# Kernel optimization log

Measured on AMD Instinct MI355X. Metric: run time of the kernel, lower is better.

The kernel has to match this reference:

```python
import jax, jax.numpy as jnp
import numpy as np

BATCH = 2048
DIMS = [256, 256, 256, 128]  # input, hidden, hidden, output
N_ATOMS = 4  # identity, sin, tanh, square


def setup_inputs() -> dict:
    key = jax.random.key(0)
    ks = jax.random.split(key, 8)
    inp = {"x": jax.random.normal(ks[0], (BATCH, DIMS[0]), dtype=jnp.float32)}
    for li in range(3):
        out_d, in_d = DIMS[li + 1], DIMS[li]
        inp[f"W{li}"] = jax.random.normal(ks[1 + li], (out_d, in_d), dtype=jnp.float32) * 0.1
        inp[f"b{li}"] = jnp.zeros((out_d,), dtype=jnp.float32)
        inp[f"f_idx{li}"] = jax.random.randint(ks[4 + li], (out_d, in_d), 0, N_ATOMS, dtype=jnp.int32)
    return inp


def _w_eff(W, idx):
    # per-element atom nonlinearity selected by idx: [identity, sin, tanh, square]
    atoms = jnp.stack([W, jnp.sin(W), jnp.tanh(W), W * W], axis=0)  # [A, out, in]
    return jnp.take_along_axis(atoms, idx[None].astype(jnp.int32), axis=0)[0]


def reference(x, W0, b0, W1, b1, W2, b2, f_idx0, f_idx1, f_idx2):
    layers = [(W0, b0, f_idx0), (W1, b1, f_idx1), (W2, b2, f_idx2)]
    h = x
    n = len(layers)
    for li, (W, b, idx) in enumerate(layers):
        We = _w_eff(W, idx)                       # [out, in]
        z = h[:, None, :] * We[None, :, :]        # [batch, out, in]
        gz = z if li == n - 1 else jnp.tanh(z)    # g_fixed='tanh' on hidden layers
        h = gz.sum(axis=-1) + b[None, :]          # [batch, out]
    return h
```

## Files before the change

### kernel.cpp

```cpp
#include <hip/hip_runtime.h>
#include <math.h>


typedef float v2f __attribute__((ext_vector_type(2)));

#define SC   2.885390081777927f
#define INV  (1.0f / 2.885390081777927f)
#define INV2PI 0.15915494309189535f
#define HS_CLAMP 32.0f
#define C8   0.00390625f

__device__ __forceinline__ float fast_rcp(float x)  { return __builtin_amdgcn_rcpf(x); }
__device__ __forceinline__ float fast_exp2(float x) { return __builtin_amdgcn_exp2f(x); }
__device__ __forceinline__ v2f pk2(float a, float b) { v2f r; r.x = a; r.y = b; return r; }

__device__ __forceinline__ v2f pk_add(v2f a, v2f b) {
    v2f d; asm("v_pk_add_f32 %0, %1, %2" : "=v"(d) : "v"(a), "v"(b)); return d;
}
__device__ __forceinline__ v2f pk_mul(v2f a, v2f b) {
    v2f d; asm("v_pk_mul_f32 %0, %1, %2" : "=v"(d) : "v"(a), "v"(b)); return d;
}
__device__ __forceinline__ v2f pk_fma(v2f a, v2f b, v2f c) {
    v2f d; asm("v_pk_fma_f32 %0, %1, %2, %3" : "=v"(d) : "v"(a), "v"(b), "v"(c)); return d;
}
__device__ __forceinline__ v2f pk_fma_lo(v2f a, v2f s, v2f c) {
    v2f d; asm("v_pk_fma_f32 %0, %1, %2, %3 op_sel_hi:[1,0,1]"
               : "=v"(d) : "v"(a), "v"(s), "v"(c)); return d;
}
__device__ __forceinline__ v2f pk_fma_hi(v2f a, v2f s, v2f c) {
    v2f d; asm("v_pk_fma_f32 %0, %1, %2, %3 op_sel:[0,1,0] op_sel_hi:[1,1,1]"
               : "=v"(d) : "v"(a), "v"(s), "v"(c)); return d;
}
__device__ __forceinline__ v2f pk_exp(v2f t) {
    v2f e; e.x = fast_exp2(t.x); e.y = fast_exp2(t.y); return e;
}
__device__ __forceinline__ v2f lo2(float4 w) { return pk2(w.x, w.y); }
__device__ __forceinline__ v2f hi2(float4 w) { return pk2(w.z, w.w); }

__global__ void weff_kernel(const float* __restrict__ W0, const int* __restrict__ I0,
                            const float* __restrict__ W1, const int* __restrict__ I1,
                            const float* __restrict__ W2, const int* __restrict__ I2,
                            float* __restrict__ ws) {
    int tid = blockIdx.x * blockDim.x + threadIdx.x;
    const float* W; const int* I; float* out; int outd; int e;
    if (tid < 65536)        { W = W0; I = I0; out = ws;          outd = 256; e = tid; }
    else if (tid < 131072)  { W = W1; I = I1; out = ws + 65536;  outd = 256; e = tid - 65536; }
    else if (tid < 163840)  { W = W2; I = I2; out = ws + 131072; outd = 128; e = tid - 131072; }
    else return;
    int o = e >> 8;
    int i = e & 255;
    float w = W[e];
    int idx = I[e];
    float sn = __builtin_amdgcn_sinf(w * INV2PI);
    float th = 1.0f - 2.0f * fast_rcp(fast_exp2(w * SC) + 1.0f);
    float sq = w * w;
    float v = (idx == 1) ? sn : (idx == 2) ? th : (idx == 3) ? sq : w;
    out[(i >> 2) * (outd * 4) + o * 4 + (i & 3)] = v;
}

struct ND { v2f n, d; };
__device__ __forceinline__ ND tree4(float4 pa, float4 pb, float4 w, v2f m8, v2f c8) {
    v2f h0 = pk2(pa.x, pa.y), h1 = pk2(pa.z, pa.w);
    v2f h2 = pk2(pb.x, pb.y), h3 = pk2(pb.z, pb.w);
    v2f wxy = lo2(w), wzw = hi2(w);
    v2f B0 = pk_add(pk_exp(pk_fma_lo(h0, wxy, m8)), c8);
    v2f B1 = pk_add(pk_exp(pk_fma_hi(h1, wxy, m8)), c8);
    v2f B2 = pk_add(pk_exp(pk_fma_lo(h2, wzw, m8)), c8);
    v2f B3 = pk_add(pk_exp(pk_fma_hi(h3, wzw, m8)), c8);
    v2f S1 = pk_add(B0, B1), P1 = pk_mul(B0, B1);
    v2f S2 = pk_add(B2, B3), P2 = pk_mul(B2, B3);
    ND r;
    r.n = pk_fma(S2, P1, pk_mul(S1, P2));
    r.d = pk_mul(P1, P2);
    return r;
}

__device__ __forceinline__ v2f sig8_acc(ND a, ND b, v2f acc) {
    v2f num = pk_fma(b.n, a.d, pk_mul(a.n, b.d));
    v2f den = pk_mul(a.d, b.d);
    v2f rd;  rd.x = fast_rcp(den.x); rd.y = fast_rcp(den.y);
    return pk_fma(num, rd, acc);
}

__global__ __launch_bounds__(512, 8) void mlp_kernel(
    const float* __restrict__ x,  const float* __restrict__ b0,
    const float* __restrict__ b1, const float* __restrict__ b2,
    const float* __restrict__ ws, float* __restrict__ out) {
    const float4* We0 = (const float4*)ws;
    const float4* We1 = (const float4*)(ws + 65536);
    const float4* We2 = (const float4*)(ws + 131072);

    __shared__ __align__(16) v2f hA[256];
    __shared__ __align__(16) v2f hB[256];
    __shared__ __align__(16) v2f part[512];

    const int t = threadIdx.x;
    const int g = t >> 8;
    const int o = t & 255;
    const int row0 = blockIdx.x * 2;

    const v2f m8 = pk2(-8.0f, -8.0f);
    const v2f c8 = pk2(C8, C8);

    {
        float xv = x[(row0 + g) * 256 + o] * SC;
        xv = fminf(fmaxf(xv, -HS_CLAMP), HS_CLAMP);
        ((float*)(hA + o))[g] = xv;
    }
    __syncthreads();

    {
        v2f acc = pk2(0.f, 0.f);
#pragma unroll 2
        for (int icc = 0; icc < 32; icc += 2) {
            int ic = g * 32 + icc;
            float4 w0 = We0[ic * 256 + o];
            float4 w1 = We0[(ic + 1) * 256 + o];
            const float4* hp = (const float4*)(hA + ic * 4);
            ND r0 = tree4(hp[0], hp[1], w0, m8, c8);
            ND r1 = tree4(hp[2], hp[3], w1, m8, c8);
            acc = sig8_acc(r0, r1, acc);
        }
        part[g * 256 + o] = acc;
        __syncthreads();
        float s = ((const float*)(part + o))[g] + ((const float*)(part + 256 + o))[g];
        float h = (256.0f - 0.0078125f * s + b0[o]) * SC;
        h = fminf(fmaxf(h, -HS_CLAMP), HS_CLAMP);
        ((float*)(hB + o))[g] = h;
        __syncthreads();
    }

    {
        v2f acc = pk2(0.f, 0.f);
#pragma unroll 2
        for (int icc = 0; icc < 32; icc += 2) {
            int ic = g * 32 + icc;
            float4 w0 = We1[ic * 256 + o];
            float4 w1 = We1[(ic + 1) * 256 + o];
            const float4* hp = (const float4*)(hB + ic * 4);
            ND r0 = tree4(hp[0], hp[1], w0, m8, c8);
            ND r1 = tree4(hp[2], hp[3], w1, m8, c8);
            acc = sig8_acc(r0, r1, acc);
        }
        part[g * 256 + o] = acc;
        __syncthreads();
        float s = ((const float*)(part + o))[g] + ((const float*)(part + 256 + o))[g];
        float h = (256.0f - 0.0078125f * s + b1[o]) * SC;
        h = fminf(fmaxf(h, -HS_CLAMP), HS_CLAMP);
        ((float*)(hA + o))[g] = h;
        __syncthreads();
    }

    {
        const int o2 = t & 127;
        const int q  = t >> 7;
        v2f acc = pk2(0.f, 0.f);
#pragma unroll 4
        for (int icc = 0; icc < 16; icc++) {
            int ic = q * 16 + icc;
            float4 w = We2[ic * 128 + o2];
            const float4* hp = (const float4*)(hA + ic * 4);
            float4 pa = hp[0], pb = hp[1];
            v2f h0 = pk2(pa.x, pa.y), h1 = pk2(pa.z, pa.w);
            v2f h2 = pk2(pb.x, pb.y), h3 = pk2(pb.z, pb.w);
            v2f wxy = lo2(w), wzw = hi2(w);
            acc = pk_fma_lo(h0, wxy, acc);
            acc = pk_fma_hi(h1, wxy, acc);
            acc = pk_fma_lo(h2, wzw, acc);
            acc = pk_fma_hi(h3, wzw, acc);
        }
        part[q * 128 + o2] = acc;
        __syncthreads();
        if (t < 256) {
            int r = t >> 7, oo = t & 127;
            float s = ((const float*)(part + oo))[r]
                    + ((const float*)(part + 128 + oo))[r]
                    + ((const float*)(part + 256 + oo))[r]
                    + ((const float*)(part + 384 + oo))[r];
            out[(row0 + r) * 128 + oo] = s * INV + b2[oo];
        }
    }
}

extern "C" void kernel_launch(void* const* d_in, const int* in_sizes, int n_in,
                              void* d_out, int out_size, void* d_ws, size_t ws_size,
                              hipStream_t stream) {
    const float* x  = (const float*)d_in[0];
    const float* W0 = (const float*)d_in[1];
    const float* b0 = (const float*)d_in[2];
    const int*   I0 = (const int*)  d_in[3];
    const float* W1 = (const float*)d_in[4];
    const float* b1 = (const float*)d_in[5];
    const int*   I1 = (const int*)  d_in[6];
    const float* W2 = (const float*)d_in[7];
    const float* b2 = (const float*)d_in[8];
    const int*   I2 = (const int*)  d_in[9];
    float* ws  = (float*)d_ws;
    float* out = (float*)d_out;

    weff_kernel<<<640, 256, 0, stream>>>(W0, I0, W1, I1, W2, I2, ws);
    mlp_kernel<<<1024, 512, 0, stream>>>(x, b0, b1, b2, ws, out);
}
```

Baseline: 115.4 us.

## Process four rows per block to reuse weight loads across two row pairs

Each block now handles four batch rows instead of two. Every float4 of effective weights loaded from global memory is applied to both row pairs, with separate shared activation and partial-sum buffers for each pair. The grid is halved and the launch bound drops to four blocks per SM to leave room for the extra registers. This halves weight traffic per output, but it raises register pressure, lowers the number of resident waves and leaves fewer blocks to spread across CUs.

```diff
diff --git a/kernel.cpp b/kernel.cpp
--- a/kernel.cpp
+++ b/kernel.cpp
@@ -82,7 +82,7 @@
     return pk_fma(num, rd, acc);
 }
 
-__global__ __launch_bounds__(512, 8) void mlp_kernel(
+__global__ __launch_bounds__(512, 4) void mlp_kernel(
     const float* __restrict__ x,  const float* __restrict__ b0,
     const float* __restrict__ b1, const float* __restrict__ b2,
     const float* __restrict__ ws, float* __restrict__ out) {
@@ -90,14 +90,17 @@
     const float4* We1 = (const float4*)(ws + 65536);
     const float4* We2 = (const float4*)(ws + 131072);
 
-    __shared__ __align__(16) v2f hA[256];
-    __shared__ __align__(16) v2f hB[256];
-    __shared__ __align__(16) v2f part[512];
+    __shared__ __align__(16) v2f hA0[256];
+    __shared__ __align__(16) v2f hA1[256];
+    __shared__ __align__(16) v2f hB0[256];
+    __shared__ __align__(16) v2f hB1[256];
+    __shared__ __align__(16) v2f partA[512];
+    __shared__ __align__(16) v2f partB[512];
 
     const int t = threadIdx.x;
     const int g = t >> 8;
     const int o = t & 255;
-    const int row0 = blockIdx.x * 2;
+    const int row0 = blockIdx.x * 4;
 
     const v2f m8 = pk2(-8.0f, -8.0f);
     const v2f c8 = pk2(C8, C8);
@@ -105,80 +108,109 @@
     {
         float xv = x[(row0 + g) * 256 + o] * SC;
         xv = fminf(fmaxf(xv, -HS_CLAMP), HS_CLAMP);
-        ((float*)(hA + o))[g] = xv;
+        ((float*)&hA0[o])[g] = xv;
+        float xw = x[(row0 + 2 + g) * 256 + o] * SC;
+        xw = fminf(fmaxf(xw, -HS_CLAMP), HS_CLAMP);
+        ((float*)&hA1[o])[g] = xw;
     }
     __syncthreads();
 
     {
-        v2f acc = pk2(0.f, 0.f);
+        const float bias = b0[o];
+        v2f acc0 = pk2(0.f, 0.f), acc1 = pk2(0.f, 0.f);
 #pragma unroll 2
         for (int icc = 0; icc < 32; icc += 2) {
             int ic = g * 32 + icc;
             float4 w0 = We0[ic * 256 + o];
             float4 w1 = We0[(ic + 1) * 256 + o];
-            const float4* hp = (const float4*)(hA + ic * 4);
-            ND r0 = tree4(hp[0], hp[1], w0, m8, c8);
-            ND r1 = tree4(hp[2], hp[3], w1, m8, c8);
-            acc = sig8_acc(r0, r1, acc);
+            const float4* hp0 = (const float4*)(hA0 + ic * 4);
+            const float4* hp1 = (const float4*)(hA1 + ic * 4);
+            ND r0 = tree4(hp0[0], hp0[1], w0, m8, c8);
+            ND r1 = tree4(hp0[2], hp0[3], w1, m8, c8);
+            acc0 = sig8_acc(r0, r1, acc0);
+            ND r2 = tree4(hp1[0], hp1[1], w0, m8, c8);
+            ND r3 = tree4(hp1[2], hp1[3], w1, m8, c8);
+            acc1 = sig8_acc(r2, r3, acc1);
         }
-        part[g * 256 + o] = acc;
-        __syncthreads();
-        float s = ((const float*)(part + o))[g] + ((const float*)(part + 256 + o))[g];
-        float h = (256.0f - 0.0078125f * s + b0[o]) * SC;
-        h = fminf(fmaxf(h, -HS_CLAMP), HS_CLAMP);
-        ((float*)(hB + o))[g] = h;
-        __syncthreads();
-    }
-
-    {
-        v2f acc = pk2(0.f, 0.f);
+        partA[g * 256 + o] = acc0;
+        partB[g * 256 + o] = acc1;
+        __syncthreads();
+        float s0 = ((const float*)(partA + o))[g] + ((const float*)(partA + 256 + o))[g];
+        float h0 = (256.0f - 0.0078125f * s0 + bias) * SC;
+        h0 = fminf(fmaxf(h0, -HS_CLAMP), HS_CLAMP);
+        ((float*)&hB0[o])[g] = h0;
+        float s1 = ((const float*)(partB + o))[g] + ((const float*)(partB + 256 + o))[g];
+        float h1 = (256.0f - 0.0078125f * s1 + bias) * SC;
+        h1 = fminf(fmaxf(h1, -HS_CLAMP), HS_CLAMP);
+        ((float*)&hB1[o])[g] = h1;
+        __syncthreads();
+    }
+
+    {
+        const float bias = b1[o];
+        v2f acc0 = pk2(0.f, 0.f), acc1 = pk2(0.f, 0.f);
 #pragma unroll 2
         for (int icc = 0; icc < 32; icc += 2) {
             int ic = g * 32 + icc;
             float4 w0 = We1[ic * 256 + o];
             float4 w1 = We1[(ic + 1) * 256 + o];
-            const float4* hp = (const float4*)(hB + ic * 4);
-            ND r0 = tree4(hp[0], hp[1], w0, m8, c8);
-            ND r1 = tree4(hp[2], hp[3], w1, m8, c8);
-            acc = sig8_acc(r0, r1, acc);
+            const float4* hp0 = (const float4*)(hB0 + ic * 4);
+            const float4* hp1 = (const float4*)(hB1 + ic * 4);
+            ND r0 = tree4(hp0[0], hp0[1], w0, m8, c8);
+            ND r1 = tree4(hp0[2], hp0[3], w1, m8, c8);
+            acc0 = sig8_acc(r0, r1, acc0);
+            ND r2 = tree4(hp1[0], hp1[1], w0, m8, c8);
+            ND r3 = tree4(hp1[2], hp1[3], w1, m8, c8);
+            acc1 = sig8_acc(r2, r3, acc1);
         }
-        part[g * 256 + o] = acc;
-        __syncthreads();
-        float s = ((const float*)(part + o))[g] + ((const float*)(part + 256 + o))[g];
-        float h = (256.0f - 0.0078125f * s + b1[o]) * SC;
-        h = fminf(fmaxf(h, -HS_CLAMP), HS_CLAMP);
-        ((float*)(hA + o))[g] = h;
+        partA[g * 256 + o] = acc0;
+        partB[g * 256 + o] = acc1;
+        __syncthreads();
+        float s0 = ((const float*)(partA + o))[g] + ((const float*)(partA + 256 + o))[g];
+        float h0 = (256.0f - 0.0078125f * s0 + bias) * SC;
+        h0 = fminf(fmaxf(h0, -HS_CLAMP), HS_CLAMP);
+        ((float*)&hA0[o])[g] = h0;
+        float s1 = ((const float*)(partB + o))[g] + ((const float*)(partB + 256 + o))[g];
+        float h1 = (256.0f - 0.0078125f * s1 + bias) * SC;
+        h1 = fminf(fmaxf(h1, -HS_CLAMP), HS_CLAMP);
+        ((float*)&hB1[o])[g] = h1;
         __syncthreads();
     }
 
     {
         const int o2 = t & 127;
         const int q  = t >> 7;
-        v2f acc = pk2(0.f, 0.f);
+        v2f acc0 = pk2(0.f, 0.f), acc1 = pk2(0.f, 0.f);
 #pragma unroll 4
         for (int icc = 0; icc < 16; icc++) {
             int ic = q * 16 + icc;
             float4 w = We2[ic * 128 + o2];
-            const float4* hp = (const float4*)(hA + ic * 4);
-            float4 pa = hp[0], pb = hp[1];
-            v2f h0 = pk2(pa.x, pa.y), h1 = pk2(pa.z, pa.w);
-            v2f h2 = pk2(pb.x, pb.y), h3 = pk2(pb.z, pb.w);
+            const float4* hp0 = (const float4*)(hA0 + ic * 4);
+            const float4* hp1 = (const float4*)(hB1 + ic * 4);
+            float4 pa = hp0[0], pb = hp0[1];
+            float4 qa = hp1[0], qb = hp1[1];
             v2f wxy = lo2(w), wzw = hi2(w);
-            acc = pk_fma_lo(h0, wxy, acc);
-            acc = pk_fma_hi(h1, wxy, acc);
-            acc = pk_fma_lo(h2, wzw, acc);
-            acc = pk_fma_hi(h3, wzw, acc);
+            acc0 = pk_fma_lo(pk2(pa.x, pa.y), wxy, acc0);
+            acc0 = pk_fma_hi(pk2(pa.z, pa.w), wxy, acc0);
+            acc0 = pk_fma_lo(pk2(pb.x, pb.y), wzw, acc0);
+            acc0 = pk_fma_hi(pk2(pb.z, pb.w), wzw, acc0);
+            acc1 = pk_fma_lo(pk2(qa.x, qa.y), wxy, acc1);
+            acc1 = pk_fma_hi(pk2(qa.z, qa.w), wxy, acc1);
+            acc1 = pk_fma_lo(pk2(qb.x, qb.y), wzw, acc1);
+            acc1 = pk_fma_hi(pk2(qb.z, qb.w), wzw, acc1);
         }
-        part[q * 128 + o2] = acc;
-        __syncthreads();
-        if (t < 256) {
-            int r = t >> 7, oo = t & 127;
-            float s = ((const float*)(part + oo))[r]
-                    + ((const float*)(part + 128 + oo))[r]
-                    + ((const float*)(part + 256 + oo))[r]
-                    + ((const float*)(part + 384 + oo))[r];
-            out[(row0 + r) * 128 + oo] = s * INV + b2[oo];
-        }
+        partA[q * 128 + o2] = acc0;
+        partB[q * 128 + o2] = acc1;
+        __syncthreads();
+        const int r  = t >> 7;
+        const int oo = t & 127;
+        const v2f* prt = (r & 2) ? partB : partA;
+        const int  ln  = r & 1;
+        float s = ((const float*)(prt + oo))[ln]
+                + ((const float*)(prt + 128 + oo))[ln]
+                + ((const float*)(prt + 256 + oo))[ln]
+                + ((const float*)(prt + 384 + oo))[ln];
+        out[(row0 + r) * 128 + oo] = s * INV + b2[oo];
     }
 }
 
@@ -199,5 +231,5 @@
     float* out = (float*)d_out;
 
     weff_kernel<<<640, 256, 0, stream>>>(W0, I0, W1, I1, W2, I2, ws);
-    mlp_kernel<<<1024, 512, 0, stream>>>(x, b0, b1, b2, ws, out);
-}
+    mlp_kernel<<<512, 512, 0, stream>>>(x, b0, b1, b2, ws, out);
+}
```

New measurement: 113.2 us. About the same (-1.9%).
